# Kernel tuning notes

Hardware: AMD Instinct MI355X
Metric: run time of the kernel (lower is better)

Reference implementation:

```python
import jax, jax.numpy as jnp
from jax import lax
import numpy as np

B, T_IN, NF, H, T_OUT = 2048, 336, 16, 128, 168


def _gru_cell(x, h, Wih, Whh, bih, bhh):
    # PyTorch GRU cell, gate order [r, z, n]
    gi = x @ Wih.T + bih          # (B, 3H)
    gh = h @ Whh.T + bhh          # (B, 3H)
    i_r, i_z, i_n = jnp.split(gi, 3, axis=-1)
    h_r, h_z, h_n = jnp.split(gh, 3, axis=-1)
    r = jax.nn.sigmoid(i_r + h_r)
    z = jax.nn.sigmoid(i_z + h_z)
    n = jnp.tanh(i_n + r * h_n)
    return (1.0 - z) * n + z * h


def _run_gru_layer(seq_tbf, Wih, Whh, bih, bhh):
    # seq_tbf: (T, B, in_dim) -> (outputs (T,B,H), final hidden (B,H))
    h0 = jnp.zeros((seq_tbf.shape[1], H), seq_tbf.dtype)
    def step(h, xt):
        h2 = _gru_cell(xt, h, Wih, Whh, bih, bhh)
        return h2, h2
    hT, ys = lax.scan(step, h0, seq_tbf)
    return ys, hT


def setup_inputs() -> dict:
    key = jax.random.key(0)
    ks = iter(jax.random.split(key, 32))
    def w(shape, fan):
        return (jax.random.normal(next(ks), shape, jnp.float32) / np.sqrt(fan).astype(np.float32))
    inp = {"x": jax.random.normal(next(ks), (B, T_IN, NF), jnp.float32)}
    inp.update(
        enc_Wih0=w((3 * H, NF), NF), enc_Whh0=w((3 * H, H), H),
        enc_bih0=w((3 * H,), H), enc_bhh0=w((3 * H,), H),
        enc_Wih1=w((3 * H, H), H), enc_Whh1=w((3 * H, H), H),
        enc_bih1=w((3 * H,), H), enc_bhh1=w((3 * H,), H),
        dec_Wih0=w((3 * H, 1), 1), dec_Whh0=w((3 * H, H), H),
        dec_bih0=w((3 * H,), H), dec_bhh0=w((3 * H,), H),
        dec_Wih1=w((3 * H, H), H), dec_Whh1=w((3 * H, H), H),
        dec_bih1=w((3 * H,), H), dec_bhh1=w((3 * H,), H),
        fc_W1=w((H // 2, H), H), fc_b1=w((H // 2,), H),
        fc_W2=w((1, H // 2), H // 2), fc_b2=w((1,), H // 2),
    )
    return inp


def reference(x, enc_Wih0, enc_Whh0, enc_bih0, enc_bhh0,
              enc_Wih1, enc_Whh1, enc_bih1, enc_bhh1,
              dec_Wih0, dec_Whh0, dec_bih0, dec_bhh0,
              dec_Wih1, dec_Whh1, dec_bih1, dec_bhh1,
              fc_W1, fc_b1, fc_W2, fc_b2):
    b = x.shape[0]
    # --- encoder: 2-layer GRU over input sequence (eval mode: dropout off) ---
    seq = jnp.transpose(x, (1, 0, 2))                       # (T_IN, B, NF)
    ys0, h0f = _run_gru_layer(seq, enc_Wih0, enc_Whh0, enc_bih0, enc_bhh0)
    _, h1f = _run_gru_layer(ys0, enc_Wih1, enc_Whh1, enc_bih1, enc_bhh1)

    def dec_step(carry, _):
        h0, h1, inp = carry                                  # inp: (B, 1)
        h0n = _gru_cell(inp, h0, dec_Wih0, dec_Whh0, dec_bih0, dec_bhh0)
        h1n = _gru_cell(h0n, h1, dec_Wih1, dec_Whh1, dec_bih1, dec_bhh1)
        hid = jax.nn.relu(h1n @ fc_W1.T + fc_b1)
        pred = jax.nn.relu(hid @ fc_W2.T + fc_b2)            # (B, 1)
        return (h0n, h1n, pred), pred[:, 0]

    init = (h0f, h1f, jnp.zeros((b, 1), x.dtype))
    _, outs = lax.scan(dec_step, init, None, length=T_OUT)   # (T_OUT, B)
    return outs.T                                            # (B, T_OUT)
```

## Files before the change

### kernel.cpp

```cpp
#include <hip/hip_runtime.h>


typedef unsigned short ushort_t;
typedef unsigned int uint_t;
typedef __attribute__((ext_vector_type(8))) short short8;
typedef __attribute__((ext_vector_type(4))) float f32x4;
typedef __attribute__((ext_vector_type(2))) unsigned int uintx2;

#define BT   8
#define NT   512
#define HD   128
#define TIN  336
#define TOUT 168
#define NFE  16
#define NB   256

#define SC_RZ (-1.44269504089f)
#define SC_N  (-2.88539008177f)

#define OFF_EWHH0 0
#define OFF_EWIH1 6144
#define OFF_EWHH1 12288
#define OFF_DWHH0 18432
#define OFF_DWIH1 24576
#define OFF_DWHH1 30720
#define OFF_EWIH0 36864
#define OFF_FW1   38400

#define MF(a_, b_, c_) __builtin_amdgcn_mfma_f32_16x16x32_bf16((a_), (b_), (c_), 0, 0, 0)

__device__ __forceinline__ ushort_t f2bf(float f) {
    union { float f; uint_t u; } v; v.f = f;
    uint_t r = v.u + 0x7FFFu + ((v.u >> 16) & 1u);
    return (ushort_t)(r >> 16);
}
__device__ __forceinline__ ushort_t f2bf_h(float f) {
    union { float f; uint_t u; } v; v.f = f;
    return (ushort_t)((v.u + 0x8000u) >> 16);
}
__device__ __forceinline__ float sig2(float t) {
    return __builtin_amdgcn_rcpf(1.f + __builtin_amdgcn_exp2f(t));
}
__device__ __forceinline__ void barrier_lds() {
    asm volatile("s_waitcnt lgkmcnt(0)\n\ts_barrier" ::: "memory");
}

__device__ __forceinline__ void pl32swap(float& a, float& b) {
    uintx2 r = __builtin_amdgcn_permlane32_swap(
        __float_as_uint(a), __float_as_uint(b), false, false);
    a = __uint_as_float(r[0]);
    b = __uint_as_float(r[1]);
}
__device__ __forceinline__ void spread2(f32x4 v, float& e0, float& e1) {
    float a0 = v[0], a2 = v[2];
    float a1 = v[1], a3 = v[3];
    pl32swap(a0, a2);
    pl32swap(a1, a3);
    e0 = a0; e1 = a1;
}

template <int CTRL>
__device__ __forceinline__ float dpp_add(float acc) {
    int x = __builtin_amdgcn_update_dpp(0, __float_as_int(acc), CTRL, 0xF, 0xF, true);
    return acc + __int_as_float(x);
}
__device__ __forceinline__ float sum16(float v) {
    v = dpp_add<0xB1>(v);
    v = dpp_add<0x4E>(v);
    v = dpp_add<0x124>(v);
    v = dpp_add<0x128>(v);
    return v;
}

extern "C" __global__ __launch_bounds__(64)
void prep_kernel(const float* __restrict__ eWhh0, const float* __restrict__ eWih1,
                 const float* __restrict__ eWhh1, const float* __restrict__ dWhh0,
                 const float* __restrict__ dWih1, const float* __restrict__ dWhh1,
                 const float* __restrict__ eWih0, const float* __restrict__ fW1,
                 uint4* __restrict__ ws)
{
    const int g = blockIdx.x;
    const int L = threadIdx.x;
    const int n_lo = L & 15, q = L >> 4;

    const float* src; int n, kb, Ksrc, dst16; float sc;
    if (g < 576) {
        const int m = g / 96, lf = g % 96;
        const float* hs[6] = {eWhh0, eWih1, eWhh1, dWhh0, dWih1, dWhh1};
        src = hs[m];
        const int nt = lf >> 2, kf = lf & 3;
        n = nt * 16 + n_lo; kb = kf * 32 + q * 8; Ksrc = 128;
        dst16 = m * 6144 + lf * 64 + L;
        sc = (n < 2 * HD) ? SC_RZ : SC_N;
    } else if (g < 600) {
        const int nt = g - 576;
        src = eWih0; n = nt * 16 + n_lo; kb = q * 8; Ksrc = 16;
        dst16 = OFF_EWIH0 + nt * 64 + L;
        sc = (n < 2 * HD) ? SC_RZ : SC_N;
    } else {
        const int lf = g - 600;
        src = fW1; n = (lf >> 2) * 16 + n_lo; kb = (lf & 3) * 32 + q * 8; Ksrc = 128;
        dst16 = OFF_FW1 + lf * 64 + L;
        sc = 1.f;
    }

    ushort_t h[8];
    #pragma unroll
    for (int j = 0; j < 8; ++j) {
        const int k = kb + j;
        h[j] = (k < Ksrc) ? f2bf(sc * src[n * Ksrc + k]) : (ushort_t)0;
    }
    uint4 o;
    o.x = (uint_t)h[0] | ((uint_t)h[1] << 16);
    o.y = (uint_t)h[2] | ((uint_t)h[3] << 16);
    o.z = (uint_t)h[4] | ((uint_t)h[5] << 16);
    o.w = (uint_t)h[6] | ((uint_t)h[7] << 16);
    ws[dst16] = o;
}

__device__ __forceinline__ void combineS(const f32x4& gr, const f32x4& gz,
                                         const f32x4& gn_i, const f32x4& gn_h,
                                         float brz, float bzz, float bin, float bhn,
                                         float* hreg, ushort_t* wb)
{
    float r_[2], z_[2], i_[2], n_[2];
    spread2(gr,   r_[0], r_[1]);
    spread2(gz,   z_[0], z_[1]);
    spread2(gn_i, i_[0], i_[1]);
    spread2(gn_h, n_[0], n_[1]);
    #pragma unroll
    for (int e = 0; e < 2; ++e) {
        const float rg = sig2(r_[e] + brz);
        const float zg = sig2(z_[e] + bzz);
        const float ng = fmaf(2.f, sig2((i_[e] + bin) + rg * (n_[e] + bhn)), -1.f);
        const float hn = fmaf(zg, hreg[e] - ng, ng);
        hreg[e] = hn;
        wb[e * 8] = f2bf_h(hn);
    }
}

#define ENC_BODY(i_, P_) do {                                                  \
    if (t < 128 && (i_) + 1 < TIN) {                                           \
        (&xf[0][0])[(1 - (P_)) * 512 + xscat] = f2bf_h(xv);                    \
        if ((i_) + 2 < TIN) xv = x[((b0 + xr) * TIN + (i_) + 2) * NFE + xfeat];\
    }                                                                          \
    const short8 Ax = *(const short8*)&xf[P_][L * 8];                          \
    short8 Ah0[4], Ah1[4];                                                     \
    _Pragma("unroll")                                                          \
    for (int kf = 0; kf < 4; ++kf) {                                           \
        Ah0[kf] = *(const short8*)&h0f[P_][kf][L * 8];                         \
        Ah1[kf] = *(const short8*)&h1f[P_][kf][L * 8];                         \
    }                                                                          \
    f32x4 a_r  = MF(Ah0[0], Wa[0][0], zf);                                     \
    f32x4 a_z  = MF(Ah0[0], Wa[1][0], zf);                                     \
    f32x4 a_nh = MF(Ah0[0], Wa[2][0], zf);                                     \
    f32x4 br1  = MF(Ah0[0], Wb[0][0], zf);                                     \
    f32x4 bz1  = MF(Ah0[0], Wb[1][0], zf);                                     \
    f32x4 b_ni = MF(Ah0[0], Wb[2][0], zf);                                     \
    f32x4 br2  = MF(Ah1[0], Wc[0][0], zf);                                     \
    f32x4 bz2  = MF(Ah1[0], Wc[1][0], zf);                                     \
    f32x4 b_nh = MF(Ah1[0], Wc[2][0], zf);                                     \
    _Pragma("unroll")                                                          \
    for (int kf = 1; kf < 4; ++kf) {                                           \
        a_r  = MF(Ah0[kf], Wa[0][kf], a_r);                                    \
        a_z  = MF(Ah0[kf], Wa[1][kf], a_z);                                    \
        a_nh = MF(Ah0[kf], Wa[2][kf], a_nh);                                   \
        br1  = MF(Ah0[kf], Wb[0][kf], br1);                                    \
        bz1  = MF(Ah0[kf], Wb[1][kf], bz1);                                    \
        b_ni = MF(Ah0[kf], Wb[2][kf], b_ni);                                   \
        br2  = MF(Ah1[kf], Wc[0][kf], br2);                                    \
        bz2  = MF(Ah1[kf], Wc[1][kf], bz2);                                    \
        b_nh = MF(Ah1[kf], Wc[2][kf], b_nh);                                   \
    }                                                                          \
    a_r = MF(Ax, We[0], a_r);                                                  \
    a_z = MF(Ax, We[1], a_z);                                                  \
    f32x4 a_ni = MF(Ax, We[2], zf);                                            \
    const f32x4 b_r = br1 + br2;                                               \
    const f32x4 b_z = bz1 + bz2;                                               \
    combineS(a_r, a_z, a_ni, a_nh, e0_rz, e0_zz, e0_in, e0_hn, h0r,            \
             &(&h0f[0][0][0])[(1 - (P_)) * 2048 + hwoE]);                      \
    combineS(b_r, b_z, b_ni, b_nh, e1_rz, e1_zz, e1_in, e1_hn, h1r,            \
             &(&h1f[0][0][0])[(1 - (P_)) * 2048 + hwoE]);                      \
    barrier_lds();                                                             \
} while (0)

#define DEC_BODY(s_, P_, Q_) do {                                              \
    {              \
        short8 Ai[4], Ah[4];                                                   \
        _Pragma("unroll")                                                      \
        for (int kf = 0; kf < 4; ++kf) {                                       \
            Ai[kf] = *(const short8*)&h0f[P_][kf][L * 8];                      \
            Ah[kf] = *(const short8*)&h1f[Q_][kf][L * 8];                      \
        }                                                                      \
        f32x4 gr1 = MF(Ai[0], Wb[0][0], zf);                                   \
        f32x4 gz1 = MF(Ai[0], Wb[1][0], zf);                                   \
        f32x4 gni = MF(Ai[0], Wb[2][0], zf);                                   \
        f32x4 gr2 = MF(Ah[0], Wc[0][0], zf);                                   \
        f32x4 gz2 = MF(Ah[0], Wc[1][0], zf);                                   \
        f32x4 gnh = MF(Ah[0], Wc[2][0], zf);                                   \
        _Pragma("unroll")                                                      \
        for (int kf = 1; kf < 4; ++kf) {                                       \
            gr1 = MF(Ai[kf], Wb[0][kf], gr1);                                  \
            gz1 = MF(Ai[kf], Wb[1][kf], gz1);                                  \
            gni = MF(Ai[kf], Wb[2][kf], gni);                                  \
            gr2 = MF(Ah[kf], Wc[0][kf], gr2);                                  \
            gz2 = MF(Ah[kf], Wc[1][kf], gz2);                                  \
            gnh = MF(Ah[kf], Wc[2][kf], gnh);                                  \
        }                                                                      \
        const f32x4 gr = gr1 + gr2;                                            \
        const f32x4 gz = gz1 + gz2;                                            \
        combineS(gr, gz, gni, gnh, d1_rz, d1_zz, d1_in, d1_hn, h1r,            \
                 &(&h1f[0][0][0])[(P_) * 2048 + hwoE]);                        \
    }                                                                          \
    barrier_lds();                                                             \
    {                              \
        short8 Af[4], Ah[4];                                                   \
        _Pragma("unroll")                                                      \
        for (int kf = 0; kf < 4; ++kf) {                                       \
            Af[kf] = *(const short8*)&h1f[P_][kf][L * 8];                      \
            Ah[kf] = *(const short8*)&h0f[P_][kf][L * 8];                      \
        }                                                                      \
        f32x4 g0 = MF(Ah[0], Wa[0][0], zf);                                    \
        f32x4 g1 = MF(Ah[0], Wa[1][0], zf);                                    \
        f32x4 g2 = MF(Ah[0], Wa[2][0], zf);                                    \
        f32x4 fc[4];                                                           \
        _Pragma("unroll")                                                      \
        for (int nt = 0; nt < 4; ++nt)                                         \
            fc[nt] = MF(Af[0], *(const short8*)&fw1l[(nt * 4) * 64 + L], zf);  \
        _Pragma("unroll")                                                      \
        for (int kf = 1; kf < 4; ++kf) {                                       \
            g0 = MF(Ah[kf], Wa[0][kf], g0);                                    \
            g1 = MF(Ah[kf], Wa[1][kf], g1);                                    \
            g2 = MF(Ah[kf], Wa[2][kf], g2);                                    \
            _Pragma("unroll")                                                  \
            for (int nt = 0; nt < 4; ++nt) {                                   \
                const short8 bfr = *(const short8*)&fw1l[(nt * 4 + kf) * 64 + L]; \
                fc[nt] = MF(Af[kf], bfr, fc[nt]);                              \
            }                                                                  \
        }                                                                      \
        float g0e[2], g1e[2], g2e[2], fe0[4], fe1[4];                          \
        _Pragma("unroll")                                                      \
        for (int nt = 0; nt < 4; ++nt) spread2(fc[nt], fe0[nt], fe1[nt]);      \
        float ps[2];                                                           \
        _Pragma("unroll")                                                      \
        for (int e = 0; e < 2; ++e) {                                          \
            float s2_ = 0.f;                                                   \
            _Pragma("unroll")                                                  \
            for (int nt = 0; nt < 4; ++nt) {                                   \
                const float v = (e == 0) ? fe0[nt] : fe1[nt];                  \
                s2_ = fmaf(fmaxf(v + f1bv[nt], 0.f), w2v[nt], s2_);            \
            }                                                                  \
            ps[e] = s2_;                                                       \
        }                                                                      \
        _Pragma("unroll")                                                      \
        for (int e = 0; e < 2; ++e) {                                          \
            ps[e] = sum16(ps[e]);                                              \
            ivr[e] = fmaxf(ps[e] + fb2v, 0.f);                                 \
        }                                                                      \
        spread2(g0, g0e[0], g0e[1]);                                           \
        spread2(g1, g1e[0], g1e[1]);                                           \
        spread2(g2, g2e[0], g2e[1]);                                           \
        if (w == 0 && col16 == 0) {                                            \
            _Pragma("unroll")                                                  \
            for (int e = 0; e < 2; ++e)                                        \
                out[(b0 + (q & 1) * 4 + hi2 + e) * TOUT + (s_)] = ivr[e];      \
        }                                                                      \
        ushort_t* wbp = &(&h0f[0][0][0])[(Q_) * 2048 + hwoE];                  \
        _Pragma("unroll")                                                      \
        for (int e = 0; e < 2; ++e) {                                          \
            const float iv = ivr[e];                                           \
            const float rg = sig2(fmaf(iv, w0r, g0e[e] + d0_rz));              \
            const float zg = sig2(fmaf(iv, w0z, g1e[e] + d0_zz));              \
            const float tt = fmaf(iv, w0n, d0_in) + rg * (g2e[e] + d0_hn);     \
            const float ng = fmaf(2.f, sig2(tt), -1.f);                        \
            const float hn = fmaf(zg, h0r[e] - ng, ng);                        \
            h0r[e] = hn;                                                       \
            wbp[e * 8] = f2bf_h(hn);                                           \
        }                                                                      \
    }                                                                          \
    barrier_lds();                                                             \
} while (0)

extern "C" __global__ __launch_bounds__(NT, 2)
void gru_seq2seq_kernel(
    const float* __restrict__ x,
    const float* __restrict__ ebih0, const float* __restrict__ ebhh0,
    const float* __restrict__ ebih1, const float* __restrict__ ebhh1,
    const float* __restrict__ dWih0, const float* __restrict__ dbih0,
    const float* __restrict__ dbhh0,
    const float* __restrict__ dbih1, const float* __restrict__ dbhh1,
    const float* __restrict__ fb1, const float* __restrict__ fW2,
    const float* __restrict__ fb2,
    const short8* __restrict__ wf,
    float* __restrict__ out)
{
    __shared__ ushort_t h0f[2][4][512];
    __shared__ ushort_t h1f[2][4][512];
    __shared__ ushort_t xf[2][512];
    __shared__ uint4 fw1l[1024];

    const int t = threadIdx.x;
    const int L = t & 63, w = t >> 6;
    const int col16 = L & 15, q = L >> 4;
    const int col = w * 16 + col16;
    const int b0 = blockIdx.x * BT;

    for (int i = t; i < 4096; i += NT) {
        (&h0f[0][0][0])[i] = 0;
        (&h1f[0][0][0])[i] = 0;
    }
    for (int i = t; i < 1024; i += NT) (&xf[0][0])[i] = 0;

    const int kfc = col >> 5, qq = (col >> 3) & 3, jc = col & 7;
    const int hi2 = (L >> 5) * 2;
    const int hwoE = kfc * 512 + (qq * 16 + (q & 1) * 4 + hi2) * 8 + jc;

    const int xr = t >> 4, xfeat = t & 15;
    const int xscat = (((xfeat >> 3) * 16) + (xr & 15)) * 8 + (xfeat & 7);
    float xv = (t < 128) ? x[((b0 + xr) * TIN + 0) * NFE + xfeat] : 0.f;

    const float e0_rz = SC_RZ * (ebih0[col] + ebhh0[col]);
    const float e0_zz = SC_RZ * (ebih0[HD + col] + ebhh0[HD + col]);
    const float e0_in = SC_N * ebih0[2 * HD + col];
    const float e0_hn = SC_N * ebhh0[2 * HD + col];
    const float e1_rz = SC_RZ * (ebih1[col] + ebhh1[col]);
    const float e1_zz = SC_RZ * (ebih1[HD + col] + ebhh1[HD + col]);
    const float e1_in = SC_N * ebih1[2 * HD + col];
    const float e1_hn = SC_N * ebhh1[2 * HD + col];

    float h0r[2] = {0, 0};
    float h1r[2] = {0, 0};

    const f32x4 zf = {0.f, 0.f, 0.f, 0.f};

    short8 Wa[3][4], Wb[3][4], Wc[3][4];
    short8 We[3];
    #pragma unroll
    for (int t3 = 0; t3 < 3; ++t3) {
        const int nt = w + t3 * 8;
        We[t3] = wf[OFF_EWIH0 + nt * 64 + L];
        #pragma unroll
        for (int kf = 0; kf < 4; ++kf) {
            Wa[t3][kf] = wf[OFF_EWHH0 + (nt * 4 + kf) * 64 + L];
            Wb[t3][kf] = wf[OFF_EWIH1 + (nt * 4 + kf) * 64 + L];
            Wc[t3][kf] = wf[OFF_EWHH1 + (nt * 4 + kf) * 64 + L];
        }
    }

    barrier_lds();
    if (t < 128) {
        (&xf[0][0])[xscat] = f2bf_h(xv);
        xv = x[((b0 + xr) * TIN + 1) * NFE + xfeat];
    }
    barrier_lds();

    {
        if (t < 128) {
            (&xf[0][0])[512 + xscat] = f2bf_h(xv);
            xv = x[((b0 + xr) * TIN + 2) * NFE + xfeat];
        }
        const short8 Ax = *(const short8*)&xf[0][L * 8];
        short8 Ah[4];
        #pragma unroll
        for (int kf = 0; kf < 4; ++kf)
            Ah[kf] = *(const short8*)&h0f[0][kf][L * 8];
        f32x4 gr  = MF(Ah[0], Wa[0][0], zf);
        f32x4 gz  = MF(Ah[0], Wa[1][0], zf);
        f32x4 gnh = MF(Ah[0], Wa[2][0], zf);
        #pragma unroll
        for (int kf = 1; kf < 4; ++kf) {
            gr  = MF(Ah[kf], Wa[0][kf], gr);
            gz  = MF(Ah[kf], Wa[1][kf], gz);
            gnh = MF(Ah[kf], Wa[2][kf], gnh);
        }
        gr = MF(Ax, We[0], gr);
        gz = MF(Ax, We[1], gz);
        f32x4 gni = MF(Ax, We[2], zf);
        combineS(gr, gz, gni, gnh, e0_rz, e0_zz, e0_in, e0_hn, h0r,
                 &(&h0f[0][0][0])[2048 + hwoE]);
        barrier_lds();
    }

    for (int i = 1; i + 1 < TIN; i += 2) {
        ENC_BODY(i, 1);
        ENC_BODY(i + 1, 0);
    }
    ENC_BODY(TIN - 1, 1);

    {
        short8 Ai[4], Ah[4];
        #pragma unroll
        for (int kf = 0; kf < 4; ++kf) {
            Ai[kf] = *(const short8*)&h0f[0][kf][L * 8];
            Ah[kf] = *(const short8*)&h1f[0][kf][L * 8];
        }
        f32x4 gr1 = MF(Ai[0], Wb[0][0], zf);
        f32x4 gz1 = MF(Ai[0], Wb[1][0], zf);
        f32x4 gni = MF(Ai[0], Wb[2][0], zf);
        f32x4 gr2 = MF(Ah[0], Wc[0][0], zf);
        f32x4 gz2 = MF(Ah[0], Wc[1][0], zf);
        f32x4 gnh = MF(Ah[0], Wc[2][0], zf);
        #pragma unroll
        for (int kf = 1; kf < 4; ++kf) {
            gr1 = MF(Ai[kf], Wb[0][kf], gr1);
            gz1 = MF(Ai[kf], Wb[1][kf], gz1);
            gni = MF(Ai[kf], Wb[2][kf], gni);
            gr2 = MF(Ah[kf], Wc[0][kf], gr2);
            gz2 = MF(Ah[kf], Wc[1][kf], gz2);
            gnh = MF(Ah[kf], Wc[2][kf], gnh);
        }
        const f32x4 gr = gr1 + gr2;
        const f32x4 gz = gz1 + gz2;
        combineS(gr, gz, gni, gnh, e1_rz, e1_zz, e1_in, e1_hn, h1r,
                 &(&h1f[0][0][0])[2048 + hwoE]);
        barrier_lds();
    }

    asm volatile("" ::: "memory");

    #pragma unroll
    for (int t3 = 0; t3 < 3; ++t3) {
        const int nt = w + t3 * 8;
        #pragma unroll
        for (int kf = 0; kf < 4; ++kf) {
            Wa[t3][kf] = wf[OFF_DWHH0 + (nt * 4 + kf) * 64 + L];
            Wb[t3][kf] = wf[OFF_DWIH1 + (nt * 4 + kf) * 64 + L];
            Wc[t3][kf] = wf[OFF_DWHH1 + (nt * 4 + kf) * 64 + L];
        }
    }
    for (int i = t; i < 1024; i += NT) fw1l[i] = ((const uint4*)wf)[OFF_FW1 + i];

    const float d0_rz = SC_RZ * (dbih0[col] + dbhh0[col]);
    const float d0_zz = SC_RZ * (dbih0[HD + col] + dbhh0[HD + col]);
    const float d0_in = SC_N * dbih0[2 * HD + col];
    const float d0_hn = SC_N * dbhh0[2 * HD + col];
    const float d1_rz = SC_RZ * (dbih1[col] + dbhh1[col]);
    const float d1_zz = SC_RZ * (dbih1[HD + col] + dbhh1[HD + col]);
    const float d1_in = SC_N * dbih1[2 * HD + col];
    const float d1_hn = SC_N * dbhh1[2 * HD + col];
    const float w0r = SC_RZ * dWih0[col];
    const float w0z = SC_RZ * dWih0[HD + col];
    const float w0n = SC_N * dWih0[2 * HD + col];
    float f1bv[4], w2v[4];
    #pragma unroll
    for (int nt = 0; nt < 4; ++nt) {
        f1bv[nt] = fb1[nt * 16 + col16];
        w2v[nt]  = fW2[nt * 16 + col16];
    }
    const float fb2v = fb2[0];
    float ivr[2] = {0.f, 0.f};

    {
        short8 Ah[4];
        #pragma unroll
        for (int kf = 0; kf < 4; ++kf)
            Ah[kf] = *(const short8*)&h0f[0][kf][L * 8];
        f32x4 g0 = MF(Ah[0], Wa[0][0], zf);
        f32x4 g1 = MF(Ah[0], Wa[1][0], zf);
        f32x4 g2 = MF(Ah[0], Wa[2][0], zf);
        #pragma unroll
        for (int kf = 1; kf < 4; ++kf) {
            g0 = MF(Ah[kf], Wa[0][kf], g0);
            g1 = MF(Ah[kf], Wa[1][kf], g1);
            g2 = MF(Ah[kf], Wa[2][kf], g2);
        }
        float g0e[2], g1e[2], g2e[2];
        spread2(g0, g0e[0], g0e[1]);
        spread2(g1, g1e[0], g1e[1]);
        spread2(g2, g2e[0], g2e[1]);
        barrier_lds();
        ushort_t* wbp = &(&h0f[0][0][0])[0 + hwoE];
        #pragma unroll
        for (int e = 0; e < 2; ++e) {
            const float rg = sig2(g0e[e] + d0_rz);
            const float zg = sig2(g1e[e] + d0_zz);
            const float ng = fmaf(2.f, sig2(d0_in + rg * (g2e[e] + d0_hn)), -1.f);
            const float hn = fmaf(zg, h0r[e] - ng, ng);
            h0r[e] = hn;
            wbp[e * 8] = f2bf_h(hn);
        }
    }
    barrier_lds();

    for (int s = 0; s < TOUT; s += 2) {
        DEC_BODY(s, 0, 1);
        DEC_BODY(s + 1, 1, 0);
    }
}

extern "C" void kernel_launch(void* const* d_in, const int* in_sizes, int n_in,
                              void* d_out, int out_size, void* d_ws, size_t ws_size,
                              hipStream_t stream) {
    const float* x     = (const float*)d_in[0];
    const float* eWih0 = (const float*)d_in[1];
    const float* eWhh0 = (const float*)d_in[2];
    const float* ebih0 = (const float*)d_in[3];
    const float* ebhh0 = (const float*)d_in[4];
    const float* eWih1 = (const float*)d_in[5];
    const float* eWhh1 = (const float*)d_in[6];
    const float* ebih1 = (const float*)d_in[7];
    const float* ebhh1 = (const float*)d_in[8];
    const float* dWih0 = (const float*)d_in[9];
    const float* dWhh0 = (const float*)d_in[10];
    const float* dbih0 = (const float*)d_in[11];
    const float* dbhh0 = (const float*)d_in[12];
    const float* dWih1 = (const float*)d_in[13];
    const float* dWhh1 = (const float*)d_in[14];
    const float* dbih1 = (const float*)d_in[15];
    const float* dbhh1 = (const float*)d_in[16];
    const float* fW1   = (const float*)d_in[17];
    const float* fb1   = (const float*)d_in[18];
    const float* fW2   = (const float*)d_in[19];
    const float* fb2   = (const float*)d_in[20];
    float* out = (float*)d_out;

    hipLaunchKernelGGL(prep_kernel, dim3(616), dim3(64), 0, stream,
                       eWhh0, eWih1, eWhh1, dWhh0, dWih1, dWhh1, eWih0, fW1,
                       (uint4*)d_ws);
    hipLaunchKernelGGL(gru_seq2seq_kernel, dim3(NB), dim3(NT), 0, stream,
                       x, ebih0, ebhh0, ebih1, ebhh1,
                       dWih0, dbih0, dbhh0, dbih1, dbhh1,
                       fb1, fW2, fb2,
                       (const short8*)d_ws, out);
}
```

Baseline: 742.6 us.

## Interleave GRU gate epilogues with MFMA chains and hoist decoder layer-0 hh matmul

The encoder step now orders the MFMA chains gate by gate and interleaves the layer-0 sigmoid/tanh epilogue with the remaining layer-1 MFMAs, so VALU/transcendental work overlaps matrix-core latency. In the decoder, the layer-0 hidden matmul (g0,g1,g2) is moved before the barrier into the first phase, reusing the already loaded h0 fragments, and the FC chain is reordered with spreads interleaved. This shortens the critical path per timestep but relies on the compiler keeping this schedule, and it raises register pressure because more accumulators are live at once.

```diff
diff --git a/kernel.cpp b/kernel.cpp
--- a/kernel.cpp
+++ b/kernel.cpp
@@ -151,96 +151,146 @@
         Ah0[kf] = *(const short8*)&h0f[P_][kf][L * 8];                         \
         Ah1[kf] = *(const short8*)&h1f[P_][kf][L * 8];                         \
     }                                                                          \
-    f32x4 a_r  = MF(Ah0[0], Wa[0][0], zf);                                     \
-    f32x4 a_z  = MF(Ah0[0], Wa[1][0], zf);                                     \
+    ushort_t* wbA = &(&h0f[0][0][0])[(1 - (P_)) * 2048 + hwoE];                \
+    ushort_t* wbB = &(&h1f[0][0][0])[(1 - (P_)) * 2048 + hwoE];                \
+                                           \
+    f32x4 a_r = MF(Ah0[0], Wa[0][0], zf);                                      \
+    a_r = MF(Ah0[1], Wa[0][1], a_r); a_r = MF(Ah0[2], Wa[0][2], a_r);          \
+    a_r = MF(Ah0[3], Wa[0][3], a_r); a_r = MF(Ax, We[0], a_r);                 \
+    f32x4 a_z = MF(Ah0[0], Wa[1][0], zf);                                      \
+    a_z = MF(Ah0[1], Wa[1][1], a_z); a_z = MF(Ah0[2], Wa[1][2], a_z);          \
+    a_z = MF(Ah0[3], Wa[1][3], a_z); a_z = MF(Ax, We[1], a_z);                 \
     f32x4 a_nh = MF(Ah0[0], Wa[2][0], zf);                                     \
-    f32x4 br1  = MF(Ah0[0], Wb[0][0], zf);                                     \
-    f32x4 bz1  = MF(Ah0[0], Wb[1][0], zf);                                     \
+    a_nh = MF(Ah0[1], Wa[2][1], a_nh); a_nh = MF(Ah0[2], Wa[2][2], a_nh);      \
+    a_nh = MF(Ah0[3], Wa[2][3], a_nh);                                         \
+    f32x4 a_ni = MF(Ax, We[2], zf);                                            \
+                                            \
+    f32x4 br1 = MF(Ah0[0], Wb[0][0], zf);                                      \
+    br1 = MF(Ah0[1], Wb[0][1], br1); br1 = MF(Ah0[2], Wb[0][2], br1);          \
+    br1 = MF(Ah0[3], Wb[0][3], br1);                                           \
+    float ar_[2], az_[2];                                                      \
+    spread2(a_r, ar_[0], ar_[1]);                                              \
+    spread2(a_z, az_[0], az_[1]);                                              \
+    f32x4 bz1 = MF(Ah0[0], Wb[1][0], zf);                                      \
+    bz1 = MF(Ah0[1], Wb[1][1], bz1); bz1 = MF(Ah0[2], Wb[1][2], bz1);          \
+    bz1 = MF(Ah0[3], Wb[1][3], bz1);                                           \
+    float ai_[2], an_[2];                                                      \
+    spread2(a_ni, ai_[0], ai_[1]);                                             \
+    spread2(a_nh, an_[0], an_[1]);                                             \
     f32x4 b_ni = MF(Ah0[0], Wb[2][0], zf);                                     \
-    f32x4 br2  = MF(Ah1[0], Wc[0][0], zf);                                     \
-    f32x4 bz2  = MF(Ah1[0], Wc[1][0], zf);                                     \
+    b_ni = MF(Ah0[1], Wb[2][1], b_ni); b_ni = MF(Ah0[2], Wb[2][2], b_ni);      \
+    b_ni = MF(Ah0[3], Wb[2][3], b_ni);                                         \
+    const float rg0 = sig2(ar_[0] + e0_rz);                                    \
+    const float zg0 = sig2(az_[0] + e0_zz);                                    \
+    f32x4 br2 = MF(Ah1[0], Wc[0][0], zf);                                      \
+    br2 = MF(Ah1[1], Wc[0][1], br2); br2 = MF(Ah1[2], Wc[0][2], br2);          \
+    br2 = MF(Ah1[3], Wc[0][3], br2);                                           \
+    {                                                                          \
+        const float ng = fmaf(2.f, sig2((ai_[0] + e0_in) + rg0 * (an_[0] + e0_hn)), -1.f); \
+        const float hn = fmaf(zg0, h0r[0] - ng, ng);                           \
+        h0r[0] = hn; wbA[0] = f2bf_h(hn);                                      \
+    }                                                                          \
+    f32x4 bz2 = MF(Ah1[0], Wc[1][0], zf);                                      \
+    bz2 = MF(Ah1[1], Wc[1][1], bz2); bz2 = MF(Ah1[2], Wc[1][2], bz2);          \
+    bz2 = MF(Ah1[3], Wc[1][3], bz2);                                           \
+    const float rg1 = sig2(ar_[1] + e0_rz);                                    \
+    const float zg1 = sig2(az_[1] + e0_zz);                                    \
     f32x4 b_nh = MF(Ah1[0], Wc[2][0], zf);                                     \
-    _Pragma("unroll")                                                          \
-    for (int kf = 1; kf < 4; ++kf) {                                           \
-        a_r  = MF(Ah0[kf], Wa[0][kf], a_r);                                    \
-        a_z  = MF(Ah0[kf], Wa[1][kf], a_z);                                    \
-        a_nh = MF(Ah0[kf], Wa[2][kf], a_nh);                                   \
-        br1  = MF(Ah0[kf], Wb[0][kf], br1);                                    \
-        bz1  = MF(Ah0[kf], Wb[1][kf], bz1);                                    \
-        b_ni = MF(Ah0[kf], Wb[2][kf], b_ni);                                   \
-        br2  = MF(Ah1[kf], Wc[0][kf], br2);                                    \
-        bz2  = MF(Ah1[kf], Wc[1][kf], bz2);                                    \
-        b_nh = MF(Ah1[kf], Wc[2][kf], b_nh);                                   \
+    b_nh = MF(Ah1[1], Wc[2][1], b_nh); b_nh = MF(Ah1[2], Wc[2][2], b_nh);      \
+    b_nh = MF(Ah1[3], Wc[2][3], b_nh);                                         \
+    {                                                                          \
+        const float ng = fmaf(2.f, sig2((ai_[1] + e0_in) + rg1 * (an_[1] + e0_hn)), -1.f); \
+        const float hn = fmaf(zg1, h0r[1] - ng, ng);                           \
+        h0r[1] = hn; wbA[8] = f2bf_h(hn);                                      \
     }                                                                          \
-    a_r = MF(Ax, We[0], a_r);                                                  \
-    a_z = MF(Ax, We[1], a_z);                                                  \
-    f32x4 a_ni = MF(Ax, We[2], zf);                                            \
     const f32x4 b_r = br1 + br2;                                               \
     const f32x4 b_z = bz1 + bz2;                                               \
-    combineS(a_r, a_z, a_ni, a_nh, e0_rz, e0_zz, e0_in, e0_hn, h0r,            \
-             &(&h0f[0][0][0])[(1 - (P_)) * 2048 + hwoE]);                      \
-    combineS(b_r, b_z, b_ni, b_nh, e1_rz, e1_zz, e1_in, e1_hn, h1r,            \
-             &(&h1f[0][0][0])[(1 - (P_)) * 2048 + hwoE]);                      \
+    combineS(b_r, b_z, b_ni, b_nh, e1_rz, e1_zz, e1_in, e1_hn, h1r, wbB);      \
     barrier_lds();                                                             \
 } while (0)
 
 #define DEC_BODY(s_, P_, Q_) do {                                              \
-    {              \
+    {                                                        \
         short8 Ai[4], Ah[4];                                                   \
         _Pragma("unroll")                                                      \
         for (int kf = 0; kf < 4; ++kf) {                                       \
             Ai[kf] = *(const short8*)&h0f[P_][kf][L * 8];                      \
             Ah[kf] = *(const short8*)&h1f[Q_][kf][L * 8];                      \
         }                                                                      \
+        ushort_t* wbB = &(&h1f[0][0][0])[(P_) * 2048 + hwoE];                  \
         f32x4 gr1 = MF(Ai[0], Wb[0][0], zf);                                   \
+        gr1 = MF(Ai[1], Wb[0][1], gr1); gr1 = MF(Ai[2], Wb[0][2], gr1);        \
+        gr1 = MF(Ai[3], Wb[0][3], gr1);                                        \
         f32x4 gz1 = MF(Ai[0], Wb[1][0], zf);                                   \
+        gz1 = MF(Ai[1], Wb[1][1], gz1); gz1 = MF(Ai[2], Wb[1][2], gz1);        \
+        gz1 = MF(Ai[3], Wb[1][3], gz1);                                        \
         f32x4 gni = MF(Ai[0], Wb[2][0], zf);                                   \
+        gni = MF(Ai[1], Wb[2][1], gni); gni = MF(Ai[2], Wb[2][2], gni);        \
+        gni = MF(Ai[3], Wb[2][3], gni);                                        \
         f32x4 gr2 = MF(Ah[0], Wc[0][0], zf);                                   \
+        gr2 = MF(Ah[1], Wc[0][1], gr2); gr2 = MF(Ah[2], Wc[0][2], gr2);        \
+        gr2 = MF(Ah[3], Wc[0][3], gr2);                                        \
         f32x4 gz2 = MF(Ah[0], Wc[1][0], zf);                                   \
+        gz2 = MF(Ah[1], Wc[1][1], gz2); gz2 = MF(Ah[2], Wc[1][2], gz2);        \
+        gz2 = MF(Ah[3], Wc[1][3], gz2);                                        \
         f32x4 gnh = MF(Ah[0], Wc[2][0], zf);                                   \
+        gnh = MF(Ah[1], Wc[2][1], gnh); gnh = MF(Ah[2], Wc[2][2], gnh);        \
+        gnh = MF(Ah[3], Wc[2][3], gnh);                                        \
+                                  \
+        g0 = MF(Ai[0], Wa[0][0], zf);                                          \
+        g0 = MF(Ai[1], Wa[0][1], g0); g0 = MF(Ai[2], Wa[0][2], g0);            \
+        g0 = MF(Ai[3], Wa[0][3], g0);                                          \
+        const f32x4 grv = gr1 + gr2;                                           \
+        const f32x4 gzv = gz1 + gz2;                                           \
+        float r_[2], z_[2];                                                    \
+        spread2(grv, r_[0], r_[1]);                                            \
+        spread2(gzv, z_[0], z_[1]);                                            \
+        g1 = MF(Ai[0], Wa[1][0], zf);                                          \
+        g1 = MF(Ai[1], Wa[1][1], g1); g1 = MF(Ai[2], Wa[1][2], g1);            \
+        g1 = MF(Ai[3], Wa[1][3], g1);                                          \
+        float i_[2], n_[2];                                                    \
+        spread2(gni, i_[0], i_[1]);                                            \
+        spread2(gnh, n_[0], n_[1]);                                            \
+        g2 = MF(Ai[0], Wa[2][0], zf);                                          \
+        g2 = MF(Ai[1], Wa[2][1], g2); g2 = MF(Ai[2], Wa[2][2], g2);            \
+        g2 = MF(Ai[3], Wa[2][3], g2);                                          \
         _Pragma("unroll")                                                      \
-        for (int kf = 1; kf < 4; ++kf) {                                       \
-            gr1 = MF(Ai[kf], Wb[0][kf], gr1);                                  \
-            gz1 = MF(Ai[kf], Wb[1][kf], gz1);                                  \
-            gni = MF(Ai[kf], Wb[2][kf], gni);                                  \
-            gr2 = MF(Ah[kf], Wc[0][kf], gr2);                                  \
-            gz2 = MF(Ah[kf], Wc[1][kf], gz2);                                  \
-            gnh = MF(Ah[kf], Wc[2][kf], gnh);                                  \
+        for (int e = 0; e < 2; ++e) {                                          \
+            const float rg = sig2(r_[e] + d1_rz);                              \
+            const float zg = sig2(z_[e] + d1_zz);                              \
+            const float ng = fmaf(2.f, sig2((i_[e] + d1_in) + rg * (n_[e] + d1_hn)), -1.f); \
+            const float hn = fmaf(zg, h1r[e] - ng, ng);                        \
+            h1r[e] = hn;                                                       \
+            wbB[e * 8] = f2bf_h(hn);                                           \
         }                                                                      \
-        const f32x4 gr = gr1 + gr2;                                            \
-        const f32x4 gz = gz1 + gz2;                                            \
-        combineS(gr, gz, gni, gnh, d1_rz, d1_zz, d1_in, d1_hn, h1r,            \
-                 &(&h1f[0][0][0])[(P_) * 2048 + hwoE]);                        \
     }                                                                          \
     barrier_lds();                                                             \
-    {                              \
-        short8 Af[4], Ah[4];                                                   \
+    {                                                        \
+        short8 Af[4];                                                          \
         _Pragma("unroll")                                                      \
-        for (int kf = 0; kf < 4; ++kf) {                                       \
+        for (int kf = 0; kf < 4; ++kf)                                         \
             Af[kf] = *(const short8*)&h1f[P_][kf][L * 8];                      \
-            Ah[kf] = *(const short8*)&h0f[P_][kf][L * 8];                      \
-        }                                                                      \
-        f32x4 g0 = MF(Ah[0], Wa[0][0], zf);                                    \
-        f32x4 g1 = MF(Ah[0], Wa[1][0], zf);                                    \
-        f32x4 g2 = MF(Ah[0], Wa[2][0], zf);                                    \
-        f32x4 fc[4];                                                           \
-        _Pragma("unroll")                                                      \
-        for (int nt = 0; nt < 4; ++nt)                                         \
-            fc[nt] = MF(Af[0], *(const short8*)&fw1l[(nt * 4) * 64 + L], zf);  \
-        _Pragma("unroll")                                                      \
-        for (int kf = 1; kf < 4; ++kf) {                                       \
-            g0 = MF(Ah[kf], Wa[0][kf], g0);                                    \
-            g1 = MF(Ah[kf], Wa[1][kf], g1);                                    \
-            g2 = MF(Ah[kf], Wa[2][kf], g2);                                    \
-            _Pragma("unroll")                                                  \
-            for (int nt = 0; nt < 4; ++nt) {                                   \
-                const short8 bfr = *(const short8*)&fw1l[(nt * 4 + kf) * 64 + L]; \
-                fc[nt] = MF(Af[kf], bfr, fc[nt]);                              \
-            }                                                                  \
-        }                                                                      \
-        float g0e[2], g1e[2], g2e[2], fe0[4], fe1[4];                          \
-        _Pragma("unroll")                                                      \
-        for (int nt = 0; nt < 4; ++nt) spread2(fc[nt], fe0[nt], fe1[nt]);      \
+        float fe0[4], fe1[4];                                                  \
+        f32x4 fc0 = MF(Af[0], *(const short8*)&fw1l[(0 * 4 + 0) * 64 + L], zf);\
+        fc0 = MF(Af[1], *(const short8*)&fw1l[(0 * 4 + 1) * 64 + L], fc0);     \
+        fc0 = MF(Af[2], *(const short8*)&fw1l[(0 * 4 + 2) * 64 + L], fc0);     \
+        fc0 = MF(Af[3], *(const short8*)&fw1l[(0 * 4 + 3) * 64 + L], fc0);     \
+        f32x4 fc1 = MF(Af[0], *(const short8*)&fw1l[(1 * 4 + 0) * 64 + L], zf);\
+        fc1 = MF(Af[1], *(const short8*)&fw1l[(1 * 4 + 1) * 64 + L], fc1);     \
+        fc1 = MF(Af[2], *(const short8*)&fw1l[(1 * 4 + 2) * 64 + L], fc1);     \
+        fc1 = MF(Af[3], *(const short8*)&fw1l[(1 * 4 + 3) * 64 + L], fc1);     \
+        spread2(fc0, fe0[0], fe1[0]);                                          \
+        f32x4 fc2 = MF(Af[0], *(const short8*)&fw1l[(2 * 4 + 0) * 64 + L], zf);\
+        fc2 = MF(Af[1], *(const short8*)&fw1l[(2 * 4 + 1) * 64 + L], fc2);     \
+        fc2 = MF(Af[2], *(const short8*)&fw1l[(2 * 4 + 2) * 64 + L], fc2);     \
+        fc2 = MF(Af[3], *(const short8*)&fw1l[(2 * 4 + 3) * 64 + L], fc2);     \
+        spread2(fc1, fe0[1], fe1[1]);                                          \
+        f32x4 fc3 = MF(Af[0], *(const short8*)&fw1l[(3 * 4 + 0) * 64 + L], zf);\
+        fc3 = MF(Af[1], *(const short8*)&fw1l[(3 * 4 + 1) * 64 + L], fc3);     \
+        fc3 = MF(Af[2], *(const short8*)&fw1l[(3 * 4 + 2) * 64 + L], fc3);     \
+        fc3 = MF(Af[3], *(const short8*)&fw1l[(3 * 4 + 3) * 64 + L], fc3);     \
+        spread2(fc2, fe0[2], fe1[2]);                                          \
+        spread2(fc3, fe0[3], fe1[3]);                                          \
         float ps[2];                                                           \
         _Pragma("unroll")                                                      \
         for (int e = 0; e < 2; ++e) {                                          \
@@ -257,6 +307,7 @@
             ps[e] = sum16(ps[e]);                                              \
             ivr[e] = fmaxf(ps[e] + fb2v, 0.f);                                 \
         }                                                                      \
+        float g0e[2], g1e[2], g2e[2];                                          \
         spread2(g0, g0e[0], g0e[1]);                                           \
         spread2(g1, g1e[0], g1e[1]);                                           \
         spread2(g2, g2e[0], g2e[1]);                                           \
@@ -449,15 +500,16 @@
     }
     const float fb2v = fb2[0];
     float ivr[2] = {0.f, 0.f};
+    f32x4 g0, g1, g2;
 
     {
         short8 Ah[4];
         #pragma unroll
         for (int kf = 0; kf < 4; ++kf)
             Ah[kf] = *(const short8*)&h0f[0][kf][L * 8];
-        f32x4 g0 = MF(Ah[0], Wa[0][0], zf);
-        f32x4 g1 = MF(Ah[0], Wa[1][0], zf);
-        f32x4 g2 = MF(Ah[0], Wa[2][0], zf);
+        g0 = MF(Ah[0], Wa[0][0], zf);
+        g1 = MF(Ah[0], Wa[1][0], zf);
+        g2 = MF(Ah[0], Wa[2][0], zf);
         #pragma unroll
         for (int kf = 1; kf < 4; ++kf) {
             g0 = MF(Ah[kf], Wa[0][kf], g0);
```

Result: no change. 747.7 us (+0.7%).
